# Kernel optimization log

Hardware: AMD Instinct MI355X
Metric: run time of the kernel (lower is better)

Reference implementation:

```python
import jax, jax.numpy as jnp
import numpy as np

B = 64          # graphs per batch
N_NODES = 2000  # nodes per graph (model hyperparameter: FC2 in_features)
NF = 128        # node features
H = 8           # hidden_dim
OC = 8          # out_channels
NC = 2          # n_classes
DEG = 16        # avg degree
SLOPE = 0.01


def _lin_init(key, fan_in, fan_out):
    k1, k2 = jax.random.split(key)
    s = 1.0 / np.sqrt(fan_in)
    W = jax.random.uniform(k1, (fan_in, fan_out), jnp.float32, -s, s)
    b = jax.random.uniform(k2, (fan_out,), jnp.float32, -s, s)
    return W, b


def setup_inputs() -> dict:
    key = jax.random.key(0)
    ks = jax.random.split(key, 10)
    N = B * N_NODES
    E = N * DEG
    x = jax.random.normal(ks[0], (N, NF), jnp.float32)
    # graph-local random edges, offset per graph
    local = jax.random.randint(ks[1], (2, E), 0, N_NODES)
    off = jnp.repeat(jnp.arange(B, dtype=jnp.int64) * N_NODES, E // B)
    edge_index = (local + off[None, :]).astype(jnp.int64)
    batch = jnp.repeat(jnp.arange(B, dtype=jnp.int64), N_NODES)
    W1a, b1a = _lin_init(ks[2], NF, H)
    W1b, b1b = _lin_init(ks[3], H, H)
    W2a, b2a = _lin_init(ks[4], H, H)
    W2b, b2b = _lin_init(ks[5], H, OC)
    Wf1, bf1 = _lin_init(ks[6], OC, 1)
    Wf2, bf2 = _lin_init(ks[7], N_NODES, NC)
    return {"x": x, "edge_index": edge_index, "batch": batch,
            "W1a": W1a, "b1a": b1a, "W1b": W1b, "b1b": b1b,
            "W2a": W2a, "b2a": b2a, "W2b": W2b, "b2b": b2b,
            "Wf1": Wf1, "bf1": bf1, "Wf2": Wf2, "bf2": bf2}


def _lrelu(v):
    return jnp.where(v >= 0, v, SLOPE * v)


def _gin_conv(h, src, dst, Wa, ba, Wb, bb):
    N = h.shape[0]
    agg = jax.ops.segment_sum(h[src], dst, num_segments=N)  # sum_{j->i} h_j
    z = h + agg                                             # (1+eps)*h + agg, eps=0
    z = _lrelu(z @ Wa + ba)                                 # MLP linear1 + act
    return z @ Wb + bb                                      # MLP linear2 (plain last)


def reference(x, edge_index, batch, W1a, b1a, W1b, b1b, W2a, b2a, W2b, b2b,
              Wf1, bf1, Wf2, bf2):
    src, dst = edge_index[0], edge_index[1]
    h = _gin_conv(x, src, dst, W1a, b1a, W1b, b1b)
    h = _lrelu(h)  # inter-layer activation (dropout = identity at eval)
    h = _gin_conv(h, src, dst, W2a, b2a, W2b, b2b)  # [N, OC], no act after last conv
    bsz = h.shape[0] // N_NODES
    y = h.reshape(bsz, N_NODES, OC)
    y = _lrelu(y) @ Wf1 + bf1          # FC1 -> [B, n_nodes, 1]
    y = y.reshape(bsz, N_NODES)
    y = _lrelu(y) @ Wf2 + bf2          # FC2 -> [B, n_classes]
    return jax.nn.log_softmax(y, axis=1)
```

## Files before the change

### kernel.cpp

```cpp
#include <hip/hip_runtime.h>
#include <math.h>

#define NF 128
#define HD 8
#define NPG 2000
#define EPB 8000
#define NPB 500
#define SLOPE 0.01f

__device__ __forceinline__ float lrelu(float v) {
    return v > 0.0f ? v : SLOPE * v;
}

__global__ __launch_bounds__(256) void k_feat(const float* __restrict__ x,
                                              const float* __restrict__ W1a,
                                              float* __restrict__ t1, int N) {
    __shared__ float tile[64 * 132];
    __shared__ float wl[NF * HD];

    const int t = threadIdx.x;
    const size_t base = (size_t)blockIdx.x * 64;

    ((float4*)wl)[t] = ((const float4*)W1a)[t];

    const float4* xg = (const float4*)(x + base * NF);
#pragma unroll
    for (int i = 0; i < 8; ++i) {
        int f4 = t + i * 256;
        float4 v = xg[f4];
        int flat = f4 * 4;
        int n = flat >> 7;
        int k = flat & 127;
        *(float4*)(tile + n * 132 + k) = v;
    }
    __syncthreads();

    const int n = t >> 2;
    const int c0 = (t & 3) * 2;
    float acc0 = 0.0f, acc1 = 0.0f;
    const float* row = tile + n * 132;
#pragma unroll
    for (int k4 = 0; k4 < 32; ++k4) {
        float4 r = *(const float4*)(row + k4 * 4);
        int kb = k4 * 4 * HD;
        acc0 += r.x * wl[kb + c0];          acc1 += r.x * wl[kb + c0 + 1];
        acc0 += r.y * wl[kb + HD + c0];     acc1 += r.y * wl[kb + HD + c0 + 1];
        acc0 += r.z * wl[kb + 2*HD + c0];   acc1 += r.z * wl[kb + 2*HD + c0 + 1];
        acc0 += r.w * wl[kb + 3*HD + c0];   acc1 += r.w * wl[kb + 3*HD + c0 + 1];
    }
    *(float2*)(t1 + (base + n) * HD + c0) = make_float2(acc0, acc1);
}

__global__ __launch_bounds__(1024) void k_sort(const int* __restrict__ ei,
                                               int* __restrict__ gcol,
                                               int* __restrict__ rpc,
                                               int E) {
    __shared__ int cnt[NPG];
    __shared__ int srt[EPB];
    __shared__ int wtot[16], wpre[16];

    const int b = blockIdx.x;
    const int g = b >> 2;
    const int tid = threadIdx.x;
    const int lane = tid & 63;
    const int wv = tid >> 6;
    const int nodeBase = g * NPG;
    const int e0 = b * EPB;

    for (int i = tid; i < NPG; i += 1024) cnt[i] = 0;
    __syncthreads();

    for (int e = e0 + tid; e < e0 + EPB; e += 1024) {
        int dl = ei[E + e] - nodeBase;
        atomicAdd(&cnt[dl], 1);
    }
    __syncthreads();

    int c0 = 0, c1 = 0;
    if (tid < 1000) { c0 = cnt[2 * tid]; c1 = cnt[2 * tid + 1]; }
    int s = c0 + c1;
    int isc = s;
#pragma unroll
    for (int d = 1; d < 64; d <<= 1) {
        int o = __shfl_up(isc, d);
        if (lane >= d) isc += o;
    }
    if (lane == 63) wtot[wv] = isc;
    __syncthreads();
    if (wv == 0) {
        int v = (lane < 16) ? wtot[lane] : 0;
        int iv = v;
#pragma unroll
        for (int d = 1; d < 16; d <<= 1) {
            int o = __shfl_up(iv, d);
            if (lane >= d) iv += o;
        }
        if (lane < 16) wpre[lane] = iv - v;
    }
    __syncthreads();
    int excl = isc - s + wpre[wv];

    int* rpb = rpc + (size_t)b * (NPG + 1);
    if (tid < 1000) {
        cnt[2 * tid]     = excl;
        cnt[2 * tid + 1] = excl + c0;
        rpb[2 * tid]     = excl;
        rpb[2 * tid + 1] = excl + c0;
    }
    if (tid == 0) rpb[NPG] = EPB;
    __syncthreads();

    for (int e = e0 + tid; e < e0 + EPB; e += 1024) {
        int src = ei[e] - nodeBase;
        int dl = ei[E + e] - nodeBase;
        int pos = atomicAdd(&cnt[dl], 1);
        srt[pos] = src;
    }
    __syncthreads();

    int4* dst4 = (int4*)(gcol + (size_t)b * EPB);
    const int4* s4 = (const int4*)srt;
    for (int i = tid; i < EPB / 4; i += 1024) dst4[i] = s4[i];
}

__global__ __launch_bounds__(512) void k_l1(
    const float* __restrict__ t1, const int* __restrict__ rpc,
    const int* __restrict__ gcol, float* __restrict__ u,
    const float* __restrict__ b1a, const float* __restrict__ W1b,
    const float* __restrict__ b1b, const float* __restrict__ W2a)
{
    __shared__ float tbl[NPG * HD];
    __shared__ float wts[144];

    const int b = blockIdx.x;
    const int g = b >> 2;
    const int q = b & 3;
    const int tid = threadIdx.x;

    if (tid < 144) {
        float v;
        if (tid < 8)       v = b1a[tid];
        else if (tid < 72) v = W1b[tid - 8];
        else if (tid < 80) v = b1b[tid - 72];
        else               v = W2a[tid - 80];
        wts[tid] = v;
    }

    const float4* src4 = (const float4*)(t1 + (size_t)g * NPG * HD);
    float4* lo4 = (float4*)tbl;
    float4* hi4 = lo4 + NPG;
#pragma unroll
    for (int i = 0; i < 8; ++i) {
        int idx = tid + i * 512;
        if (idx < 2 * NPG) {
            float4 v = src4[idx];
            int n = idx >> 1;
            if (idx & 1) hi4[n] = v; else lo4[n] = v;
        }
    }
    __syncthreads();

    if (tid < NPB) {
        const int nl = q * NPB + tid;
        float a0 = 0, a1 = 0, a2 = 0, a3 = 0, a4 = 0, a5 = 0, a6 = 0, a7 = 0;
#pragma unroll
        for (int p = 0; p < 4; ++p) {
            const int* rpb  = rpc + (size_t)((g << 2) + p) * (NPG + 1);
            const int* colp = gcol + (size_t)((g << 2) + p) * EPB;
            int rs = rpb[nl], re = rpb[nl + 1];
            for (int e = rs; e < re; ++e) {
                int sl = colp[e];
                float4 pa = lo4[sl];
                float4 pb = hi4[sl];
                a0 += pa.x; a1 += pa.y; a2 += pa.z; a3 += pa.w;
                a4 += pb.x; a5 += pb.y; a6 += pb.z; a7 += pb.w;
            }
        }
        float4 tA = lo4[nl], tB = hi4[nl];
        float z[HD];
        z[0] = lrelu(tA.x + a0 + wts[0]); z[1] = lrelu(tA.y + a1 + wts[1]);
        z[2] = lrelu(tA.z + a2 + wts[2]); z[3] = lrelu(tA.w + a3 + wts[3]);
        z[4] = lrelu(tB.x + a4 + wts[4]); z[5] = lrelu(tB.y + a5 + wts[5]);
        z[6] = lrelu(tB.z + a6 + wts[6]); z[7] = lrelu(tB.w + a7 + wts[7]);

        float h[HD];
#pragma unroll
        for (int j = 0; j < HD; ++j) {
            float acc = wts[72 + j];
#pragma unroll
            for (int c = 0; c < HD; ++c) acc += z[c] * wts[8 + c * HD + j];
            h[j] = lrelu(acc);
        }
        float uu[HD];
#pragma unroll
        for (int j = 0; j < HD; ++j) {
            float acc = 0.0f;
#pragma unroll
            for (int c = 0; c < HD; ++c) acc += h[c] * wts[80 + c * HD + j];
            uu[j] = acc;
        }
        float* ur = u + ((size_t)g * NPG + nl) * HD;
        *(float4*)ur       = make_float4(uu[0], uu[1], uu[2], uu[3]);
        *(float4*)(ur + 4) = make_float4(uu[4], uu[5], uu[6], uu[7]);
    }
}

__global__ __launch_bounds__(512) void k_l2(
    const float* __restrict__ u, const int* __restrict__ rpc,
    const int* __restrict__ gcol,
    const float* __restrict__ b2a, const float* __restrict__ W2b,
    const float* __restrict__ b2b, const float* __restrict__ Wf1,
    const float* __restrict__ bf1, const float* __restrict__ Wf2,
    float* __restrict__ bparts)
{
    __shared__ float tbl[NPG * HD];
    __shared__ float wts[89];
    __shared__ float red[16];

    const int b = blockIdx.x;
    const int g = b >> 2;
    const int q = b & 3;
    const int tid = threadIdx.x;
    const int lane = tid & 63;
    const int wv = tid >> 6;

    if (tid < 89) {
        float v;
        if (tid < 8)       v = b2a[tid];
        else if (tid < 72) v = W2b[tid - 8];
        else if (tid < 80) v = b2b[tid - 72];
        else if (tid < 88) v = Wf1[tid - 80];
        else               v = bf1[0];
        wts[tid] = v;
    }

    const float4* src4 = (const float4*)(u + (size_t)g * NPG * HD);
    float4* lo4 = (float4*)tbl;
    float4* hi4 = lo4 + NPG;
#pragma unroll
    for (int i = 0; i < 8; ++i) {
        int idx = tid + i * 512;
        if (idx < 2 * NPG) {
            float4 v = src4[idx];
            int n = idx >> 1;
            if (idx & 1) hi4[n] = v; else lo4[n] = v;
        }
    }
    __syncthreads();

    float acc0 = 0.0f, acc1 = 0.0f;
    if (tid < NPB) {
        const int nl = q * NPB + tid;
        float a0 = 0, a1 = 0, a2 = 0, a3 = 0, a4 = 0, a5 = 0, a6 = 0, a7 = 0;
#pragma unroll
        for (int p = 0; p < 4; ++p) {
            const int* rpb  = rpc + (size_t)((g << 2) + p) * (NPG + 1);
            const int* colp = gcol + (size_t)((g << 2) + p) * EPB;
            int rs = rpb[nl], re = rpb[nl + 1];
            for (int e = rs; e < re; ++e) {
                int sl = colp[e];
                float4 pa = lo4[sl];
                float4 pb = hi4[sl];
                a0 += pa.x; a1 += pa.y; a2 += pa.z; a3 += pa.w;
                a4 += pb.x; a5 += pb.y; a6 += pb.z; a7 += pb.w;
            }
        }
        float4 uA = lo4[nl], uB = hi4[nl];
        float z[HD];
        z[0] = lrelu(uA.x + a0 + wts[0]); z[1] = lrelu(uA.y + a1 + wts[1]);
        z[2] = lrelu(uA.z + a2 + wts[2]); z[3] = lrelu(uA.w + a3 + wts[3]);
        z[4] = lrelu(uB.x + a4 + wts[4]); z[5] = lrelu(uB.y + a5 + wts[5]);
        z[6] = lrelu(uB.z + a6 + wts[6]); z[7] = lrelu(uB.w + a7 + wts[7]);

        float sv = wts[88];
#pragma unroll
        for (int j = 0; j < HD; ++j) {
            float acc = wts[72 + j];
#pragma unroll
            for (int c = 0; c < HD; ++c) acc += z[c] * wts[8 + c * HD + j];
            sv += lrelu(acc) * wts[80 + j];
        }
        float pf = lrelu(sv);
        float2 wf = *(const float2*)(Wf2 + (size_t)nl * 2);
        acc0 = pf * wf.x;
        acc1 = pf * wf.y;
    }

#pragma unroll
    for (int off = 32; off > 0; off >>= 1) {
        acc0 += __shfl_down(acc0, off);
        acc1 += __shfl_down(acc1, off);
    }
    if (lane == 0) { red[wv * 2] = acc0; red[wv * 2 + 1] = acc1; }
    __syncthreads();

    if (tid == 0) {
        float y0 = 0.f, y1 = 0.f;
#pragma unroll
        for (int w = 0; w < 8; ++w) { y0 += red[w * 2]; y1 += red[w * 2 + 1]; }
        *(float2*)(bparts + (size_t)b * 2) = make_float2(y0, y1);
    }
}

__global__ __launch_bounds__(64) void k_fin(const float* __restrict__ bparts,
                                            const float* __restrict__ bf2,
                                            float* __restrict__ out, int Bn) {
    int g = threadIdx.x;
    if (g >= Bn) return;
    float y0 = bf2[0], y1 = bf2[1];
#pragma unroll
    for (int b = 0; b < 4; ++b) {
        float2 v = *(const float2*)(bparts + (size_t)(g * 4 + b) * 2);
        y0 += v.x; y1 += v.y;
    }
    float m = fmaxf(y0, y1);
    float lse = m + logf(expf(y0 - m) + expf(y1 - m));
    out[g * 2 + 0] = y0 - lse;
    out[g * 2 + 1] = y1 - lse;
}

extern "C" void kernel_launch(void* const* d_in, const int* in_sizes, int n_in,
                              void* d_out, int out_size, void* d_ws, size_t ws_size,
                              hipStream_t stream) {
    const float* x   = (const float*)d_in[0];
    const int*   ei  = (const int*)  d_in[1];
    const float* W1a = (const float*)d_in[3];
    const float* b1a = (const float*)d_in[4];
    const float* W1b = (const float*)d_in[5];
    const float* b1b = (const float*)d_in[6];
    const float* W2a = (const float*)d_in[7];
    const float* b2a = (const float*)d_in[8];
    const float* W2b = (const float*)d_in[9];
    const float* b2b = (const float*)d_in[10];
    const float* Wf1 = (const float*)d_in[11];
    const float* bf1 = (const float*)d_in[12];
    const float* Wf2 = (const float*)d_in[13];
    const float* bf2 = (const float*)d_in[14];

    int N   = in_sizes[0] / NF;
    int E   = in_sizes[1] / 2;
    int Bn  = N / NPG;
    int NC  = Bn * 4;

    float* t1     = (float*)d_ws;
    float* u      = t1 + (size_t)N * HD;
    int*   gcol   = (int*)(u + (size_t)N * HD);
    int*   rpc    = gcol + (size_t)E;
    float* bparts = (float*)(rpc + (size_t)NC * (NPG + 1) + 16);

    k_feat <<<N / 64, 256, 0, stream>>>(x, W1a, t1, N);
    k_sort <<<NC, 1024, 0, stream>>>(ei, gcol, rpc, E);
    k_l1   <<<NC, 512, 0, stream>>>(t1, rpc, gcol, u, b1a, W1b, b1b, W2a);
    k_l2   <<<NC, 512, 0, stream>>>(u, rpc, gcol, b2a, W2b, b2b, Wf1, bf1,
                                    Wf2, bparts);
    k_fin  <<<1, 64, 0, stream>>>(bparts, bf2, (float*)d_out, Bn);
}
```

Before: 163.6 us.

## Split per-node gather across four lanes and double layer block count

The two GIN aggregation kernels now assign four threads per node, one per edge partition from the sort, and combine their partial sums with xor shuffles. Each block covers 250 nodes with 1024 threads, so there are 8 blocks per graph instead of 4. The aim is more parallelism and shorter serial gather chains per thread. In exchange, each graph's 64KB feature table is loaded into shared memory twice as often, three of every four lanes sit idle during the MLP epilogue, and the final reduction has more partials.

```diff
diff --git a/kernel.cpp b/kernel.cpp
--- a/kernel.cpp
+++ b/kernel.cpp
@@ -5,7 +5,8 @@
 #define HD 8
 #define NPG 2000
 #define EPB 8000
-#define NPB 500
+#define LPB 8
+#define LNPB 250
 #define SLOPE 0.01f
 
 __device__ __forceinline__ float lrelu(float v) {
@@ -123,7 +124,7 @@
     for (int i = tid; i < EPB / 4; i += 1024) dst4[i] = s4[i];
 }
 
-__global__ __launch_bounds__(512) void k_l1(
+__global__ __launch_bounds__(1024, 8) void k_l1(
     const float* __restrict__ t1, const int* __restrict__ rpc,
     const int* __restrict__ gcol, float* __restrict__ u,
     const float* __restrict__ b1a, const float* __restrict__ W1b,
@@ -133,8 +134,8 @@
     __shared__ float wts[144];
 
     const int b = blockIdx.x;
-    const int g = b >> 2;
-    const int q = b & 3;
+    const int g = b >> 3;
+    const int q = b & 7;
     const int tid = threadIdx.x;
 
     if (tid < 144) {
@@ -150,8 +151,8 @@
     float4* lo4 = (float4*)tbl;
     float4* hi4 = lo4 + NPG;
 #pragma unroll
-    for (int i = 0; i < 8; ++i) {
-        int idx = tid + i * 512;
+    for (int i = 0; i < 4; ++i) {
+        int idx = tid + i * 1024;
         if (idx < 2 * NPG) {
             float4 v = src4[idx];
             int n = idx >> 1;
@@ -160,52 +161,60 @@
     }
     __syncthreads();
 
-    if (tid < NPB) {
-        const int nl = q * NPB + tid;
+    if (tid < 4 * LNPB) {
+        const int node = tid >> 2;
+        const int p = tid & 3;
+        const int nl = q * LNPB + node;
+        const int* rpb  = rpc + (size_t)((g << 2) + p) * (NPG + 1);
+        const int* colp = gcol + (size_t)((g << 2) + p) * EPB;
+        int rs = rpb[nl], re = rpb[nl + 1];
         float a0 = 0, a1 = 0, a2 = 0, a3 = 0, a4 = 0, a5 = 0, a6 = 0, a7 = 0;
-#pragma unroll
-        for (int p = 0; p < 4; ++p) {
-            const int* rpb  = rpc + (size_t)((g << 2) + p) * (NPG + 1);
-            const int* colp = gcol + (size_t)((g << 2) + p) * EPB;
-            int rs = rpb[nl], re = rpb[nl + 1];
-            for (int e = rs; e < re; ++e) {
-                int sl = colp[e];
-                float4 pa = lo4[sl];
-                float4 pb = hi4[sl];
-                a0 += pa.x; a1 += pa.y; a2 += pa.z; a3 += pa.w;
-                a4 += pb.x; a5 += pb.y; a6 += pb.z; a7 += pb.w;
+        for (int e = rs; e < re; ++e) {
+            int sl = colp[e];
+            float4 pa = lo4[sl];
+            float4 pb = hi4[sl];
+            a0 += pa.x; a1 += pa.y; a2 += pa.z; a3 += pa.w;
+            a4 += pb.x; a5 += pb.y; a6 += pb.z; a7 += pb.w;
+        }
+#pragma unroll
+        for (int off = 1; off <= 2; off <<= 1) {
+            a0 += __shfl_xor(a0, off); a1 += __shfl_xor(a1, off);
+            a2 += __shfl_xor(a2, off); a3 += __shfl_xor(a3, off);
+            a4 += __shfl_xor(a4, off); a5 += __shfl_xor(a5, off);
+            a6 += __shfl_xor(a6, off); a7 += __shfl_xor(a7, off);
+        }
+        if (p == 0) {
+            float4 tA = lo4[nl], tB = hi4[nl];
+            float z[HD];
+            z[0] = lrelu(tA.x + a0 + wts[0]); z[1] = lrelu(tA.y + a1 + wts[1]);
+            z[2] = lrelu(tA.z + a2 + wts[2]); z[3] = lrelu(tA.w + a3 + wts[3]);
+            z[4] = lrelu(tB.x + a4 + wts[4]); z[5] = lrelu(tB.y + a5 + wts[5]);
+            z[6] = lrelu(tB.z + a6 + wts[6]); z[7] = lrelu(tB.w + a7 + wts[7]);
+
+            float h[HD];
+#pragma unroll
+            for (int j = 0; j < HD; ++j) {
+                float acc = wts[72 + j];
+#pragma unroll
+                for (int c = 0; c < HD; ++c) acc += z[c] * wts[8 + c * HD + j];
+                h[j] = lrelu(acc);
             }
-        }
-        float4 tA = lo4[nl], tB = hi4[nl];
-        float z[HD];
-        z[0] = lrelu(tA.x + a0 + wts[0]); z[1] = lrelu(tA.y + a1 + wts[1]);
-        z[2] = lrelu(tA.z + a2 + wts[2]); z[3] = lrelu(tA.w + a3 + wts[3]);
-        z[4] = lrelu(tB.x + a4 + wts[4]); z[5] = lrelu(tB.y + a5 + wts[5]);
-        z[6] = lrelu(tB.z + a6 + wts[6]); z[7] = lrelu(tB.w + a7 + wts[7]);
-
-        float h[HD];
-#pragma unroll
-        for (int j = 0; j < HD; ++j) {
-            float acc = wts[72 + j];
-#pragma unroll
-            for (int c = 0; c < HD; ++c) acc += z[c] * wts[8 + c * HD + j];
-            h[j] = lrelu(acc);
-        }
-        float uu[HD];
-#pragma unroll
-        for (int j = 0; j < HD; ++j) {
-            float acc = 0.0f;
-#pragma unroll
-            for (int c = 0; c < HD; ++c) acc += h[c] * wts[80 + c * HD + j];
-            uu[j] = acc;
-        }
-        float* ur = u + ((size_t)g * NPG + nl) * HD;
-        *(float4*)ur       = make_float4(uu[0], uu[1], uu[2], uu[3]);
-        *(float4*)(ur + 4) = make_float4(uu[4], uu[5], uu[6], uu[7]);
-    }
-}
-
-__global__ __launch_bounds__(512) void k_l2(
+            float uu[HD];
+#pragma unroll
+            for (int j = 0; j < HD; ++j) {
+                float acc = 0.0f;
+#pragma unroll
+                for (int c = 0; c < HD; ++c) acc += h[c] * wts[80 + c * HD + j];
+                uu[j] = acc;
+            }
+            float* ur = u + ((size_t)g * NPG + nl) * HD;
+            *(float4*)ur       = make_float4(uu[0], uu[1], uu[2], uu[3]);
+            *(float4*)(ur + 4) = make_float4(uu[4], uu[5], uu[6], uu[7]);
+        }
+    }
+}
+
+__global__ __launch_bounds__(1024, 8) void k_l2(
     const float* __restrict__ u, const int* __restrict__ rpc,
     const int* __restrict__ gcol,
     const float* __restrict__ b2a, const float* __restrict__ W2b,
@@ -215,11 +224,11 @@
 {
     __shared__ float tbl[NPG * HD];
     __shared__ float wts[89];
-    __shared__ float red[16];
+    __shared__ float red[32];
 
     const int b = blockIdx.x;
-    const int g = b >> 2;
-    const int q = b & 3;
+    const int g = b >> 3;
+    const int q = b & 7;
     const int tid = threadIdx.x;
     const int lane = tid & 63;
     const int wv = tid >> 6;
@@ -238,8 +247,8 @@
     float4* lo4 = (float4*)tbl;
     float4* hi4 = lo4 + NPG;
 #pragma unroll
-    for (int i = 0; i < 8; ++i) {
-        int idx = tid + i * 512;
+    for (int i = 0; i < 4; ++i) {
+        int idx = tid + i * 1024;
         if (idx < 2 * NPG) {
             float4 v = src4[idx];
             int n = idx >> 1;
@@ -249,41 +258,49 @@
     __syncthreads();
 
     float acc0 = 0.0f, acc1 = 0.0f;
-    if (tid < NPB) {
-        const int nl = q * NPB + tid;
+    if (tid < 4 * LNPB) {
+        const int node = tid >> 2;
+        const int p = tid & 3;
+        const int nl = q * LNPB + node;
+        const int* rpb  = rpc + (size_t)((g << 2) + p) * (NPG + 1);
+        const int* colp = gcol + (size_t)((g << 2) + p) * EPB;
+        int rs = rpb[nl], re = rpb[nl + 1];
         float a0 = 0, a1 = 0, a2 = 0, a3 = 0, a4 = 0, a5 = 0, a6 = 0, a7 = 0;
-#pragma unroll
-        for (int p = 0; p < 4; ++p) {
-            const int* rpb  = rpc + (size_t)((g << 2) + p) * (NPG + 1);
-            const int* colp = gcol + (size_t)((g << 2) + p) * EPB;
-            int rs = rpb[nl], re = rpb[nl + 1];
-            for (int e = rs; e < re; ++e) {
-                int sl = colp[e];
-                float4 pa = lo4[sl];
-                float4 pb = hi4[sl];
-                a0 += pa.x; a1 += pa.y; a2 += pa.z; a3 += pa.w;
-                a4 += pb.x; a5 += pb.y; a6 += pb.z; a7 += pb.w;
+        for (int e = rs; e < re; ++e) {
+            int sl = colp[e];
+            float4 pa = lo4[sl];
+            float4 pb = hi4[sl];
+            a0 += pa.x; a1 += pa.y; a2 += pa.z; a3 += pa.w;
+            a4 += pb.x; a5 += pb.y; a6 += pb.z; a7 += pb.w;
+        }
+#pragma unroll
+        for (int off = 1; off <= 2; off <<= 1) {
+            a0 += __shfl_xor(a0, off); a1 += __shfl_xor(a1, off);
+            a2 += __shfl_xor(a2, off); a3 += __shfl_xor(a3, off);
+            a4 += __shfl_xor(a4, off); a5 += __shfl_xor(a5, off);
+            a6 += __shfl_xor(a6, off); a7 += __shfl_xor(a7, off);
+        }
+        if (p == 0) {
+            float4 uA = lo4[nl], uB = hi4[nl];
+            float z[HD];
+            z[0] = lrelu(uA.x + a0 + wts[0]); z[1] = lrelu(uA.y + a1 + wts[1]);
+            z[2] = lrelu(uA.z + a2 + wts[2]); z[3] = lrelu(uA.w + a3 + wts[3]);
+            z[4] = lrelu(uB.x + a4 + wts[4]); z[5] = lrelu(uB.y + a5 + wts[5]);
+            z[6] = lrelu(uB.z + a6 + wts[6]); z[7] = lrelu(uB.w + a7 + wts[7]);
+
+            float sv = wts[88];
+#pragma unroll
+            for (int j = 0; j < HD; ++j) {
+                float acc = wts[72 + j];
+#pragma unroll
+                for (int c = 0; c < HD; ++c) acc += z[c] * wts[8 + c * HD + j];
+                sv += lrelu(acc) * wts[80 + j];
             }
-        }
-        float4 uA = lo4[nl], uB = hi4[nl];
-        float z[HD];
-        z[0] = lrelu(uA.x + a0 + wts[0]); z[1] = lrelu(uA.y + a1 + wts[1]);
-        z[2] = lrelu(uA.z + a2 + wts[2]); z[3] = lrelu(uA.w + a3 + wts[3]);
-        z[4] = lrelu(uB.x + a4 + wts[4]); z[5] = lrelu(uB.y + a5 + wts[5]);
-        z[6] = lrelu(uB.z + a6 + wts[6]); z[7] = lrelu(uB.w + a7 + wts[7]);
-
-        float sv = wts[88];
-#pragma unroll
-        for (int j = 0; j < HD; ++j) {
-            float acc = wts[72 + j];
-#pragma unroll
-            for (int c = 0; c < HD; ++c) acc += z[c] * wts[8 + c * HD + j];
-            sv += lrelu(acc) * wts[80 + j];
-        }
-        float pf = lrelu(sv);
-        float2 wf = *(const float2*)(Wf2 + (size_t)nl * 2);
-        acc0 = pf * wf.x;
-        acc1 = pf * wf.y;
+            float pf = lrelu(sv);
+            float2 wf = *(const float2*)(Wf2 + (size_t)nl * 2);
+            acc0 = pf * wf.x;
+            acc1 = pf * wf.y;
+        }
     }
 
 #pragma unroll
@@ -297,7 +314,7 @@
     if (tid == 0) {
         float y0 = 0.f, y1 = 0.f;
 #pragma unroll
-        for (int w = 0; w < 8; ++w) { y0 += red[w * 2]; y1 += red[w * 2 + 1]; }
+        for (int w = 0; w < 16; ++w) { y0 += red[w * 2]; y1 += red[w * 2 + 1]; }
         *(float2*)(bparts + (size_t)b * 2) = make_float2(y0, y1);
     }
 }
@@ -309,8 +326,8 @@
     if (g >= Bn) return;
     float y0 = bf2[0], y1 = bf2[1];
 #pragma unroll
-    for (int b = 0; b < 4; ++b) {
-        float2 v = *(const float2*)(bparts + (size_t)(g * 4 + b) * 2);
+    for (int b = 0; b < LPB; ++b) {
+        float2 v = *(const float2*)(bparts + (size_t)(g * LPB + b) * 2);
         y0 += v.x; y1 += v.y;
     }
     float m = fmaxf(y0, y1);
@@ -350,8 +367,8 @@
 
     k_feat <<<N / 64, 256, 0, stream>>>(x, W1a, t1, N);
     k_sort <<<NC, 1024, 0, stream>>>(ei, gcol, rpc, E);
-    k_l1   <<<NC, 512, 0, stream>>>(t1, rpc, gcol, u, b1a, W1b, b1b, W2a);
-    k_l2   <<<NC, 512, 0, stream>>>(u, rpc, gcol, b2a, W2b, b2b, Wf1, bf1,
-                                    Wf2, bparts);
+    k_l1   <<<Bn * LPB, 1024, 0, stream>>>(t1, rpc, gcol, u, b1a, W1b, b1b, W2a);
+    k_l2   <<<Bn * LPB, 1024, 0, stream>>>(u, rpc, gcol, b2a, W2b, b2b, Wf1,
+                                           bf1, Wf2, bparts);
     k_fin  <<<1, 64, 0, stream>>>(bparts, bf2, (float*)d_out, Bn);
 }
```

After: 190.5 us. +16.4%, slower.

## Merge feature projection and edge sort into one heterogeneous kernel launch

Applied to the files above, without the earlier changes.

Combines the x@W1a projection kernel and the per-chunk CSR edge sort into a single launch. The first NC blocks do the sort and the rest do the feature projection, with shared memory overlaid through a union. This removes one launch and the serialization between the two independent stages so they can overlap on the GPU. The sort now runs with 256 threads instead of 1024, each thread scanning 8 counts, which may make the sort blocks slower. The larger shared-memory footprint could also reduce occupancy for the feature blocks.

```diff
diff --git a/kernel.cpp b/kernel.cpp
--- a/kernel.cpp
+++ b/kernel.cpp
@@ -12,115 +12,120 @@
     return v > 0.0f ? v : SLOPE * v;
 }
 
-__global__ __launch_bounds__(256) void k_feat(const float* __restrict__ x,
-                                              const float* __restrict__ W1a,
-                                              float* __restrict__ t1, int N) {
-    __shared__ float tile[64 * 132];
-    __shared__ float wl[NF * HD];
+__global__ __launch_bounds__(256) void k_featsort(
+    const float* __restrict__ x, const float* __restrict__ W1a,
+    const int* __restrict__ ei, float* __restrict__ t1,
+    int* __restrict__ gcol, int* __restrict__ rpc, int N, int E, int NC)
+{
+    __shared__ union {
+        struct { float tile[64 * 132]; float wl[NF * HD]; } f;
+        struct { int cnt[NPG]; int srt[EPB]; int wtot[16]; int wpre[16]; } s;
+    } sm;
 
     const int t = threadIdx.x;
-    const size_t base = (size_t)blockIdx.x * 64;
-
-    ((float4*)wl)[t] = ((const float4*)W1a)[t];
-
-    const float4* xg = (const float4*)(x + base * NF);
-#pragma unroll
-    for (int i = 0; i < 8; ++i) {
-        int f4 = t + i * 256;
-        float4 v = xg[f4];
-        int flat = f4 * 4;
-        int n = flat >> 7;
-        int k = flat & 127;
-        *(float4*)(tile + n * 132 + k) = v;
-    }
-    __syncthreads();
-
-    const int n = t >> 2;
-    const int c0 = (t & 3) * 2;
-    float acc0 = 0.0f, acc1 = 0.0f;
-    const float* row = tile + n * 132;
-#pragma unroll
-    for (int k4 = 0; k4 < 32; ++k4) {
-        float4 r = *(const float4*)(row + k4 * 4);
-        int kb = k4 * 4 * HD;
-        acc0 += r.x * wl[kb + c0];          acc1 += r.x * wl[kb + c0 + 1];
-        acc0 += r.y * wl[kb + HD + c0];     acc1 += r.y * wl[kb + HD + c0 + 1];
-        acc0 += r.z * wl[kb + 2*HD + c0];   acc1 += r.z * wl[kb + 2*HD + c0 + 1];
-        acc0 += r.w * wl[kb + 3*HD + c0];   acc1 += r.w * wl[kb + 3*HD + c0 + 1];
-    }
-    *(float2*)(t1 + (base + n) * HD + c0) = make_float2(acc0, acc1);
-}
-
-__global__ __launch_bounds__(1024) void k_sort(const int* __restrict__ ei,
-                                               int* __restrict__ gcol,
-                                               int* __restrict__ rpc,
-                                               int E) {
-    __shared__ int cnt[NPG];
-    __shared__ int srt[EPB];
-    __shared__ int wtot[16], wpre[16];
-
-    const int b = blockIdx.x;
-    const int g = b >> 2;
-    const int tid = threadIdx.x;
-    const int lane = tid & 63;
-    const int wv = tid >> 6;
-    const int nodeBase = g * NPG;
-    const int e0 = b * EPB;
-
-    for (int i = tid; i < NPG; i += 1024) cnt[i] = 0;
-    __syncthreads();
-
-    for (int e = e0 + tid; e < e0 + EPB; e += 1024) {
-        int dl = ei[E + e] - nodeBase;
-        atomicAdd(&cnt[dl], 1);
-    }
-    __syncthreads();
-
-    int c0 = 0, c1 = 0;
-    if (tid < 1000) { c0 = cnt[2 * tid]; c1 = cnt[2 * tid + 1]; }
-    int s = c0 + c1;
-    int isc = s;
-#pragma unroll
-    for (int d = 1; d < 64; d <<= 1) {
-        int o = __shfl_up(isc, d);
-        if (lane >= d) isc += o;
-    }
-    if (lane == 63) wtot[wv] = isc;
-    __syncthreads();
-    if (wv == 0) {
-        int v = (lane < 16) ? wtot[lane] : 0;
-        int iv = v;
-#pragma unroll
-        for (int d = 1; d < 16; d <<= 1) {
-            int o = __shfl_up(iv, d);
-            if (lane >= d) iv += o;
-        }
-        if (lane < 16) wpre[lane] = iv - v;
-    }
-    __syncthreads();
-    int excl = isc - s + wpre[wv];
-
-    int* rpb = rpc + (size_t)b * (NPG + 1);
-    if (tid < 1000) {
-        cnt[2 * tid]     = excl;
-        cnt[2 * tid + 1] = excl + c0;
-        rpb[2 * tid]     = excl;
-        rpb[2 * tid + 1] = excl + c0;
-    }
-    if (tid == 0) rpb[NPG] = EPB;
-    __syncthreads();
-
-    for (int e = e0 + tid; e < e0 + EPB; e += 1024) {
-        int src = ei[e] - nodeBase;
-        int dl = ei[E + e] - nodeBase;
-        int pos = atomicAdd(&cnt[dl], 1);
-        srt[pos] = src;
-    }
-    __syncthreads();
-
-    int4* dst4 = (int4*)(gcol + (size_t)b * EPB);
-    const int4* s4 = (const int4*)srt;
-    for (int i = tid; i < EPB / 4; i += 1024) dst4[i] = s4[i];
+
+    if ((int)blockIdx.x < NC) {
+        const int b = blockIdx.x;
+        const int g = b >> 2;
+        const int lane = t & 63;
+        const int wv = t >> 6;
+        const int nodeBase = g * NPG;
+        const int e0 = b * EPB;
+
+        for (int i = t; i < NPG; i += 256) sm.s.cnt[i] = 0;
+        __syncthreads();
+
+        for (int e = e0 + t; e < e0 + EPB; e += 256) {
+            int dl = ei[E + e] - nodeBase;
+            atomicAdd(&sm.s.cnt[dl], 1);
+        }
+        __syncthreads();
+
+        int lv[8]; int s = 0;
+        if (t < 250) {
+            int base = t * 8;
+#pragma unroll
+            for (int j = 0; j < 8; ++j) { lv[j] = sm.s.cnt[base + j]; s += lv[j]; }
+        }
+        int isc = s;
+#pragma unroll
+        for (int d = 1; d < 64; d <<= 1) {
+            int o = __shfl_up(isc, d);
+            if (lane >= d) isc += o;
+        }
+        if (lane == 63) sm.s.wtot[wv] = isc;
+        __syncthreads();
+        if (wv == 0) {
+            int v = (lane < 4) ? sm.s.wtot[lane] : 0;
+            int iv = v;
+#pragma unroll
+            for (int d = 1; d < 4; d <<= 1) {
+                int o = __shfl_up(iv, d);
+                if (lane >= d) iv += o;
+            }
+            if (lane < 4) sm.s.wpre[lane] = iv - v;
+        }
+        __syncthreads();
+        int excl = isc - s + sm.s.wpre[wv];
+
+        int* rpb = rpc + (size_t)b * (NPG + 1);
+        if (t < 250) {
+            int base = t * 8;
+            int run = excl;
+#pragma unroll
+            for (int j = 0; j < 8; ++j) {
+                int idx = base + j;
+                rpb[idx] = run;
+                sm.s.cnt[idx] = run;
+                run += lv[j];
+            }
+        }
+        if (t == 0) rpb[NPG] = EPB;
+        __syncthreads();
+
+        for (int e = e0 + t; e < e0 + EPB; e += 256) {
+            int src = ei[e] - nodeBase;
+            int dl = ei[E + e] - nodeBase;
+            int pos = atomicAdd(&sm.s.cnt[dl], 1);
+            sm.s.srt[pos] = src;
+        }
+        __syncthreads();
+
+        int4* dst4 = (int4*)(gcol + (size_t)b * EPB);
+        const int4* s4 = (const int4*)sm.s.srt;
+        for (int i = t; i < EPB / 4; i += 256) dst4[i] = s4[i];
+    } else {
+        const size_t base = (size_t)(blockIdx.x - NC) * 64;
+
+        ((float4*)sm.f.wl)[t] = ((const float4*)W1a)[t];
+
+        const float4* xg = (const float4*)(x + base * NF);
+#pragma unroll
+        for (int i = 0; i < 8; ++i) {
+            int f4 = t + i * 256;
+            float4 v = xg[f4];
+            int flat = f4 * 4;
+            int n = flat >> 7;
+            int k = flat & 127;
+            *(float4*)(sm.f.tile + n * 132 + k) = v;
+        }
+        __syncthreads();
+
+        const int n = t >> 2;
+        const int c0 = (t & 3) * 2;
+        float acc0 = 0.0f, acc1 = 0.0f;
+        const float* row = sm.f.tile + n * 132;
+#pragma unroll
+        for (int k4 = 0; k4 < 32; ++k4) {
+            float4 r = *(const float4*)(row + k4 * 4);
+            int kb = k4 * 4 * HD;
+            acc0 += r.x * sm.f.wl[kb + c0];          acc1 += r.x * sm.f.wl[kb + c0 + 1];
+            acc0 += r.y * sm.f.wl[kb + HD + c0];     acc1 += r.y * sm.f.wl[kb + HD + c0 + 1];
+            acc0 += r.z * sm.f.wl[kb + 2*HD + c0];   acc1 += r.z * sm.f.wl[kb + 2*HD + c0 + 1];
+            acc0 += r.w * sm.f.wl[kb + 3*HD + c0];   acc1 += r.w * sm.f.wl[kb + 3*HD + c0 + 1];
+        }
+        *(float2*)(t1 + (base + n) * HD + c0) = make_float2(acc0, acc1);
+    }
 }
 
 __global__ __launch_bounds__(512) void k_l1(
@@ -348,10 +353,10 @@
     int*   rpc    = gcol + (size_t)E;
     float* bparts = (float*)(rpc + (size_t)NC * (NPG + 1) + 16);
 
-    k_feat <<<N / 64, 256, 0, stream>>>(x, W1a, t1, N);
-    k_sort <<<NC, 1024, 0, stream>>>(ei, gcol, rpc, E);
-    k_l1   <<<NC, 512, 0, stream>>>(t1, rpc, gcol, u, b1a, W1b, b1b, W2a);
-    k_l2   <<<NC, 512, 0, stream>>>(u, rpc, gcol, b2a, W2b, b2b, Wf1, bf1,
-                                    Wf2, bparts);
-    k_fin  <<<1, 64, 0, stream>>>(bparts, bf2, (float*)d_out, Bn);
-}
+    k_featsort<<<NC + N / 64, 256, 0, stream>>>(x, W1a, ei, t1, gcol, rpc,
+                                                N, E, NC);
+    k_l1 <<<NC, 512, 0, stream>>>(t1, rpc, gcol, u, b1a, W1b, b1b, W2a);
+    k_l2 <<<NC, 512, 0, stream>>>(u, rpc, gcol, b2a, W2b, b2b, Wf1, bf1,
+                                  Wf2, bparts);
+    k_fin<<<1, 64, 0, stream>>>(bparts, bf2, (float*)d_out, Bn);
+}
```

Result: slower. 169.3 us (+3.5%).
